# Kernel optimization log

Measured on AMD Instinct MI355X. Metric: run time of the kernel, lower is better.

Reference implementation:

```python
import jax, jax.numpy as jnp
import numpy as np

B, S, H, D = 2, 2048, 16, 64
HID = H * D
THETA = 10000.0
SCALING_FACTOR = 1
NEG_INF = -1e9


def _rope_cos_sin(position_ids):
    # Llama RoPE: inv_freq over even dims, duplicated halves.
    inv_freq = 1.0 / (THETA ** (jnp.arange(0, D, 2, dtype=jnp.float32) / D))  # [D/2]
    freqs = position_ids.astype(jnp.float32)[..., None] * inv_freq            # [B,S,D/2]
    emb = jnp.concatenate([freqs, freqs], axis=-1)                            # [B,S,D]
    return jnp.cos(emb), jnp.sin(emb)


def _rotate_half(x):
    x1, x2 = jnp.split(x, 2, axis=-1)
    return jnp.concatenate([-x2, x1], axis=-1)


def setup_inputs() -> dict:
    key = jax.random.key(0)
    ks = jax.random.split(key, 6)
    return {
        "hidden_states": jax.random.normal(ks[0], (B, S, HID), dtype=jnp.float32),
        "info_embeddings": jax.random.normal(ks[1], (B, S, HID), dtype=jnp.float32) * 0.1,
        "Wq": jax.random.normal(ks[2], (HID, HID), dtype=jnp.float32) * 0.02,
        "Wk": jax.random.normal(ks[3], (HID, HID), dtype=jnp.float32) * 0.02,
        "Wv": jax.random.normal(ks[4], (HID, HID), dtype=jnp.float32) * 0.02,
        "Wo": jax.random.normal(ks[5], (HID, HID), dtype=jnp.float32) * 0.02,
        "position_ids": jnp.broadcast_to(jnp.arange(S, dtype=jnp.int64), (B, S)),
    }


def reference(hidden_states, info_embeddings, Wq, Wk, Wv, Wo, position_ids):
    b, s, _ = hidden_states.shape
    # projections -> [B,H,S,D]
    q = (hidden_states @ Wq).reshape(b, s, H, D).transpose(0, 2, 1, 3)
    k = (hidden_states @ Wk).reshape(b, s, H, D).transpose(0, 2, 1, 3)
    v = (hidden_states @ Wv).reshape(b, s, H, D).transpose(0, 2, 1, 3)
    # info embedding added to q and k (pre-RoPE)
    info = info_embeddings.reshape(b, s, H, D).transpose(0, 2, 1, 3)
    q = q + info
    k = k + info
    # rotary position embedding
    cos, sin = _rope_cos_sin(position_ids)
    cos = cos[:, None]  # [B,1,S,D]
    sin = sin[:, None]
    q = q * cos + _rotate_half(q) * sin
    k = k * cos + _rotate_half(k) * sin
    # eager attention with custom scaling
    scale = 1.0 / float(np.sqrt(SCALING_FACTOR * D))
    scores = jnp.einsum("bhqd,bhkd->bhqk", q, k) * scale  # [B,H,S,S]
    causal = jnp.tril(jnp.ones((s, s), dtype=bool))
    scores = scores + jnp.where(causal, 0.0, NEG_INF).astype(scores.dtype)
    probs = jax.nn.softmax(scores, axis=-1)  # dropout p=0 (eval)
    attn = jnp.einsum("bhqk,bhkd->bhqd", probs, v)
    attn = attn.transpose(0, 2, 1, 3).reshape(b, s, HID)
    return attn @ Wo
```

## Files before the change

kernel.cpp:

```cpp
#include <hip/hip_runtime.h>
#include <hip/hip_bf16.h>

#define HB 2
#define HS 2048
#define HH 16
#define HD 64
#define HIDN 1024
#define MROWS 4096

typedef __attribute__((ext_vector_type(8))) short s16x8;
typedef __attribute__((ext_vector_type(4))) float f32x4;
typedef unsigned short u16;

__device__ inline u16 f2bf(float f) {
  union { __hip_bfloat16 h; u16 u; } cvt;
  cvt.h = __float2bfloat16(f);
  return cvt.u;
}

__global__ __launch_bounds__(256) void k_cvt(const float* __restrict__ in, u16* __restrict__ out, int n) {
  int i = (blockIdx.x * 256 + threadIdx.x) * 4;
  if (i >= n) return;
  float4 a = *(const float4*)(in + i);
  ushort4 r;
  r.x = f2bf(a.x); r.y = f2bf(a.y); r.z = f2bf(a.z); r.w = f2bf(a.w);
  *(ushort4*)(out + i) = r;
}

__global__ __launch_bounds__(256) void k_transpose(const float* __restrict__ W0, const float* __restrict__ W1,
                                                   const float* __restrict__ W2, const float* __restrict__ W3,
                                                   u16* __restrict__ out) {
  const float* W = (blockIdx.z == 0) ? W0 : (blockIdx.z == 1) ? W1 : (blockIdx.z == 2) ? W2 : W3;
  u16* O = out + (size_t)blockIdx.z * HIDN * HIDN;
  __shared__ float tile[64][65];
  int k0 = blockIdx.y * 64, c0 = blockIdx.x * 64;
  #pragma unroll
  for (int i = 0; i < 16; ++i) {
    int id = threadIdx.x + i * 256;
    int r = id >> 6, c = id & 63;
    tile[r][c] = W[(size_t)(k0 + r) * HIDN + c0 + c];
  }
  __syncthreads();
  #pragma unroll
  for (int i = 0; i < 16; ++i) {
    int id = threadIdx.x + i * 256;
    int r = id >> 6, c = id & 63;
    O[(size_t)(c0 + r) * HIDN + k0 + c] = f2bf(tile[c][r]);
  }
}

#define BM 128
#define BN 128
#define BK 64
#define LDK 72

__global__ __launch_bounds__(256) void k_qkv(const u16* __restrict__ X, const u16* __restrict__ Wt,
                                             const float* __restrict__ info,
                                             u16* __restrict__ Qb, u16* __restrict__ Kb, u16* __restrict__ Vt) {
  __shared__ u16 As[BM * LDK];
  __shared__ u16 Bs[BN * LDK];
  const int z = blockIdx.z;
  const u16* Bt = Wt + (size_t)z * HIDN * HIDN;
  const int tid = threadIdx.x;
  const int lane = tid & 63, wave = tid >> 6;
  const int wr = wave >> 1, wc = wave & 1;
  const int lg = lane >> 4, li = lane & 15;
  const int bm0 = blockIdx.y * BM, bn0 = blockIdx.x * BN;

  f32x4 acc[4][4];
  #pragma unroll
  for (int m = 0; m < 4; ++m)
    #pragma unroll
    for (int n = 0; n < 4; ++n) acc[m][n] = (f32x4){0.f, 0.f, 0.f, 0.f};

  for (int k0 = 0; k0 < HIDN; k0 += BK) {
    __syncthreads();
    #pragma unroll
    for (int i = 0; i < 4; ++i) {
      int id = tid + i * 256;
      int r = id >> 3, kc = (id & 7) * 8;
      *(uint4*)(&As[r * LDK + kc]) = *(const uint4*)(X  + (size_t)(bm0 + r) * HIDN + k0 + kc);
      *(uint4*)(&Bs[r * LDK + kc]) = *(const uint4*)(Bt + (size_t)(bn0 + r) * HIDN + k0 + kc);
    }
    __syncthreads();
    #pragma unroll
    for (int kk = 0; kk < 2; ++kk) {
      s16x8 af[4], bfr[4];
      #pragma unroll
      for (int m = 0; m < 4; ++m) af[m]  = *(const s16x8*)(&As[(wr * 64 + m * 16 + li) * LDK + kk * 32 + lg * 8]);
      #pragma unroll
      for (int n = 0; n < 4; ++n) bfr[n] = *(const s16x8*)(&Bs[(wc * 64 + n * 16 + li) * LDK + kk * 32 + lg * 8]);
      #pragma unroll
      for (int m = 0; m < 4; ++m)
        #pragma unroll
        for (int n = 0; n < 4; ++n)
          acc[m][n] = __builtin_amdgcn_mfma_f32_16x16x32_bf16(af[m], bfr[n], acc[m][n], 0, 0, 0);
    }
  }

  if (z < 2) {
    u16* dst = (z == 0) ? Qb : Kb;
    #pragma unroll
    for (int m = 0; m < 4; ++m) {
      #pragma unroll
      for (int r = 0; r < 4; ++r) {
        int t = bm0 + wr * 64 + m * 16 + lg * 4 + r;
        int b = t >> 11, s = t & (HS - 1);
        #pragma unroll
        for (int n = 0; n < 2; ++n) {
          int c1 = bn0 + wc * 64 + n * 16 + li;
          float v1 = acc[m][n][r]     + info[(size_t)t * HIDN + c1];
          float v2 = acc[m][n + 2][r] + info[(size_t)t * HIDN + c1 + 32];
          int j = n * 16 + li;
          float invf = exp2f(-0.41524101186092030f * (float)j);
          float ang = (float)s * invf;
          float sn, cs;
          __sincosf(ang, &sn, &cs);
          float o1 = v1 * cs - v2 * sn;
          float o2 = v2 * cs + v1 * sn;
          if (z == 0) { o1 *= 0.18033688011f; o2 *= 0.18033688011f; }
          int h = c1 >> 6, d1 = c1 & 63;
          size_t base = ((size_t)(b * HH + h) * HS + s) * HD;
          dst[base + d1]      = f2bf(o1);
          dst[base + d1 + 32] = f2bf(o2);
        }
      }
    }
  } else {
    #pragma unroll
    for (int m = 0; m < 4; ++m) {
      #pragma unroll
      for (int r = 0; r < 4; ++r) {
        int t = bm0 + wr * 64 + m * 16 + lg * 4 + r;
        int b = t >> 11, s = t & (HS - 1);
        #pragma unroll
        for (int n = 0; n < 4; ++n) {
          int c = bn0 + wc * 64 + n * 16 + li;
          int h = c >> 6, d = c & 63;
          Vt[((size_t)(b * HH + h) * HD + d) * HS + s] = f2bf(acc[m][n][r]);
        }
      }
    }
  }
}

__global__ __launch_bounds__(256) void k_attn(const u16* __restrict__ Qb, const u16* __restrict__ Kb,
                                              const u16* __restrict__ Vt, u16* __restrict__ attnOut) {
  __shared__ u16 Ks[64 * LDK];
  __shared__ u16 Vs[64 * LDK];
  __shared__ u16 Ps[4][16 * LDK];
  const int bh = blockIdx.y;
  const u16* Qh = Qb + (size_t)bh * HS * HD;
  const u16* Kh = Kb + (size_t)bh * HS * HD;
  const u16* Vh = Vt + (size_t)bh * HD * HS;
  const int tid = threadIdx.x;
  const int lane = tid & 63, wave = tid >> 6;
  const int lg = lane >> 4, li = lane & 15;
  const int b = bh >> 4, h = bh & 15;

  const int sr0 = tid >> 3,          sc0 = (tid & 7) * 8;
  const int sr1 = (tid + 256) >> 3,  sc1 = ((tid + 256) & 7) * 8;

  #pragma unroll
  for (int phase = 0; phase < 2; ++phase) {
    const int qt = (phase == 0) ? (31 - (int)blockIdx.x) : (int)blockIdx.x;
    const int q0 = qt * 64;
    const int ntiles = qt + 1;

    s16x8 qf[2];
    #pragma unroll
    for (int kk = 0; kk < 2; ++kk)
      qf[kk] = *(const s16x8*)(Qh + (size_t)(q0 + wave * 16 + li) * HD + kk * 32 + lg * 8);

    f32x4 o[4];
    #pragma unroll
    for (int n = 0; n < 4; ++n) o[n] = (f32x4){0.f, 0.f, 0.f, 0.f};
    float mrow = -3e38f, lrow = 0.f;

    uint4 rK0, rK1, rV0, rV1;
    rK0 = *(const uint4*)(Kh + (size_t)sr0 * HD + sc0);
    rK1 = *(const uint4*)(Kh + (size_t)sr1 * HD + sc1);
    rV0 = *(const uint4*)(Vh + (size_t)sr0 * HS + sc0);
    rV1 = *(const uint4*)(Vh + (size_t)sr1 * HS + sc1);

    for (int t = 0; t < ntiles; ++t) {
      __syncthreads();
      *(uint4*)(&Ks[sr0 * LDK + sc0]) = rK0;
      *(uint4*)(&Ks[sr1 * LDK + sc1]) = rK1;
      *(uint4*)(&Vs[sr0 * LDK + sc0]) = rV0;
      *(uint4*)(&Vs[sr1 * LDK + sc1]) = rV1;
      __syncthreads();
      if (t + 1 < ntiles) {
        const int kv1 = (t + 1) * 64;
        rK0 = *(const uint4*)(Kh + (size_t)(kv1 + sr0) * HD + sc0);
        rK1 = *(const uint4*)(Kh + (size_t)(kv1 + sr1) * HD + sc1);
        rV0 = *(const uint4*)(Vh + (size_t)sr0 * HS + kv1 + sc0);
        rV1 = *(const uint4*)(Vh + (size_t)sr1 * HS + kv1 + sc1);
      }

      f32x4 sc[4];
      #pragma unroll
      for (int n = 0; n < 4; ++n) sc[n] = (f32x4){0.f, 0.f, 0.f, 0.f};
      __builtin_amdgcn_s_setprio(1);
      #pragma unroll
      for (int kk = 0; kk < 2; ++kk) {
        #pragma unroll
        for (int n = 0; n < 4; ++n) {
          s16x8 kfr = *(const s16x8*)(&Ks[(n * 16 + li) * LDK + kk * 32 + lg * 8]);
          sc[n] = __builtin_amdgcn_mfma_f32_16x16x32_bf16(kfr, qf[kk], sc[n], 0, 0, 0);
        }
      }
      __builtin_amdgcn_s_setprio(0);

      if (t == ntiles - 1) {
        const int qrel = wave * 16 + li;
        #pragma unroll
        for (int n = 0; n < 4; ++n)
          #pragma unroll
          for (int r = 0; r < 4; ++r)
            if (n * 16 + lg * 4 + r > qrel) sc[n][r] = -1e9f;
      }

      float pmax = sc[0][0];
      #pragma unroll
      for (int n = 0; n < 4; ++n)
        #pragma unroll
        for (int r = 0; r < 4; ++r) pmax = fmaxf(pmax, sc[n][r]);
      pmax = fmaxf(pmax, __shfl_xor(pmax, 16));
      pmax = fmaxf(pmax, __shfl_xor(pmax, 32));

      if (!__all(pmax - mrow <= 11.5f)) {
        float mnew = fmaxf(mrow, pmax);
        float corr = exp2f(mrow - mnew);
        mrow = mnew;
        lrow *= corr;
        float corrq[4];
        #pragma unroll
        for (int r = 0; r < 4; ++r) corrq[r] = __shfl(corr, lg * 4 + r);
        #pragma unroll
        for (int n = 0; n < 4; ++n)
          #pragma unroll
          for (int r = 0; r < 4; ++r) o[n][r] *= corrq[r];
      }

      float psum = 0.f;
      #pragma unroll
      for (int n = 0; n < 4; ++n) {
        u16 pb[4];
        #pragma unroll
        for (int r = 0; r < 4; ++r) {
          float p = exp2f(sc[n][r] - mrow);
          psum += p;
          pb[r] = f2bf(p);
        }
        uint2 w;
        w.x = (unsigned)pb[0] | ((unsigned)pb[1] << 16);
        w.y = (unsigned)pb[2] | ((unsigned)pb[3] << 16);
        *(uint2*)(&Ps[wave][li * LDK + n * 16 + lg * 4]) = w;
      }
      psum += __shfl_xor(psum, 16);
      psum += __shfl_xor(psum, 32);
      lrow += psum;

      __builtin_amdgcn_s_setprio(1);
      #pragma unroll
      for (int kk = 0; kk < 2; ++kk) {
        s16x8 pf = *(const s16x8*)(&Ps[wave][li * LDK + kk * 32 + lg * 8]);
        #pragma unroll
        for (int n = 0; n < 4; ++n) {
          s16x8 vf = *(const s16x8*)(&Vs[(n * 16 + li) * LDK + kk * 32 + lg * 8]);
          o[n] = __builtin_amdgcn_mfma_f32_16x16x32_bf16(pf, vf, o[n], 0, 0, 0);
        }
      }
      __builtin_amdgcn_s_setprio(0);
    }

    float linv = 1.0f / lrow;
    float linvq[4];
    #pragma unroll
    for (int r = 0; r < 4; ++r) linvq[r] = __shfl(linv, lg * 4 + r);
    #pragma unroll
    for (int n = 0; n < 4; ++n)
      #pragma unroll
      for (int r = 0; r < 4; ++r) {
        int srow = q0 + wave * 16 + lg * 4 + r;
        attnOut[(size_t)(b * HS + srow) * HIDN + h * 64 + n * 16 + li] = f2bf(o[n][r] * linvq[r]);
      }
  }
}

__global__ __launch_bounds__(256) void k_out(const u16* __restrict__ A, const u16* __restrict__ Bt,
                                             float* __restrict__ out) {
  __shared__ u16 As[BM * LDK];
  __shared__ u16 Bs[BN * LDK];
  const int tid = threadIdx.x;
  const int lane = tid & 63, wave = tid >> 6;
  const int wr = wave >> 1, wc = wave & 1;
  const int lg = lane >> 4, li = lane & 15;
  const int bm0 = blockIdx.y * BM, bn0 = blockIdx.x * BN;

  f32x4 acc[4][4];
  #pragma unroll
  for (int m = 0; m < 4; ++m)
    #pragma unroll
    for (int n = 0; n < 4; ++n) acc[m][n] = (f32x4){0.f, 0.f, 0.f, 0.f};

  for (int k0 = 0; k0 < HIDN; k0 += BK) {
    __syncthreads();
    #pragma unroll
    for (int i = 0; i < 4; ++i) {
      int id = tid + i * 256;
      int r = id >> 3, kc = (id & 7) * 8;
      *(uint4*)(&As[r * LDK + kc]) = *(const uint4*)(A  + (size_t)(bm0 + r) * HIDN + k0 + kc);
      *(uint4*)(&Bs[r * LDK + kc]) = *(const uint4*)(Bt + (size_t)(bn0 + r) * HIDN + k0 + kc);
    }
    __syncthreads();
    #pragma unroll
    for (int kk = 0; kk < 2; ++kk) {
      s16x8 af[4], bfr[4];
      #pragma unroll
      for (int m = 0; m < 4; ++m) af[m]  = *(const s16x8*)(&As[(wr * 64 + m * 16 + li) * LDK + kk * 32 + lg * 8]);
      #pragma unroll
      for (int n = 0; n < 4; ++n) bfr[n] = *(const s16x8*)(&Bs[(wc * 64 + n * 16 + li) * LDK + kk * 32 + lg * 8]);
      #pragma unroll
      for (int m = 0; m < 4; ++m)
        #pragma unroll
        for (int n = 0; n < 4; ++n)
          acc[m][n] = __builtin_amdgcn_mfma_f32_16x16x32_bf16(af[m], bfr[n], acc[m][n], 0, 0, 0);
    }
  }

  #pragma unroll
  for (int m = 0; m < 4; ++m)
    #pragma unroll
    for (int r = 0; r < 4; ++r) {
      int t = bm0 + wr * 64 + m * 16 + lg * 4 + r;
      #pragma unroll
      for (int n = 0; n < 4; ++n) {
        int c = bn0 + wc * 64 + n * 16 + li;
        out[(size_t)t * HIDN + c] = acc[m][n][r];
      }
    }
}

extern "C" void kernel_launch(void* const* d_in, const int* in_sizes, int n_in,
                              void* d_out, int out_size, void* d_ws, size_t ws_size,
                              hipStream_t stream) {
  const float* hs   = (const float*)d_in[0];
  const float* info = (const float*)d_in[1];
  const float* Wq   = (const float*)d_in[2];
  const float* Wk   = (const float*)d_in[3];
  const float* Wv   = (const float*)d_in[4];
  const float* Wo   = (const float*)d_in[5];
  float* out = (float*)d_out;

  char* ws = (char*)d_ws;
  u16* Xbf  = (u16*)(ws);
  u16* Wt   = (u16*)(ws + ((size_t)8  << 20));
  u16* Qb   = (u16*)(ws + ((size_t)16 << 20));
  u16* Kb   = (u16*)(ws + ((size_t)24 << 20));
  u16* Vt   = (u16*)(ws + ((size_t)32 << 20));
  u16* attn = Xbf;

  k_cvt<<<(MROWS * HIDN / 4 + 255) / 256, 256, 0, stream>>>(hs, Xbf, MROWS * HIDN);
  k_transpose<<<dim3(16, 16, 4), 256, 0, stream>>>(Wq, Wk, Wv, Wo, Wt);
  k_qkv<<<dim3(HIDN / BN, MROWS / BM, 3), 256, 0, stream>>>(Xbf, Wt, info, Qb, Kb, Vt);
  k_attn<<<dim3(16, HB * HH), 256, 0, stream>>>(Qb, Kb, Vt, attn);
  k_out<<<dim3(HIDN / BN, MROWS / BM), 256, 0, stream>>>(attn, Wt + (size_t)3 * HIDN * HIDN, out);
}
```

Before: 133.5 us.

## Use direct global-to-LDS loads in GEMMs and stage V transpose through LDS

Both GEMM kernels now load tiles with global_load_lds, which writes straight into unpadded LDS rows and skips the round trip through registers. The MFMA blocks are wrapped in s_setprio to favour the math waves. The V epilogue now transposes the tile through shared memory and writes contiguous 16-byte vectors, replacing scattered 2-byte stores. The unpadded 64-element row stride may cause LDS bank conflicts on the fragment reads.

Result: faster. 127.5 us (-4.5%).

```diff
diff --git a/kernel.cpp b/kernel.cpp
--- a/kernel.cpp
+++ b/kernel.cpp
@@ -16,6 +16,11 @@
   union { __hip_bfloat16 h; u16 u; } cvt;
   cvt.h = __float2bfloat16(f);
   return cvt.u;
+}
+
+__device__ __forceinline__ void gload16(const u16* g, u16* l) {
+  __builtin_amdgcn_global_load_lds((const __attribute__((address_space(1))) void*)g,
+                                   (__attribute__((address_space(3))) void*)l, 16, 0, 0);
 }
 
 __global__ __launch_bounds__(256) void k_cvt(const float* __restrict__ in, u16* __restrict__ out, int n) {
@@ -57,8 +62,7 @@
 __global__ __launch_bounds__(256) void k_qkv(const u16* __restrict__ X, const u16* __restrict__ Wt,
                                              const float* __restrict__ info,
                                              u16* __restrict__ Qb, u16* __restrict__ Kb, u16* __restrict__ Vt) {
-  __shared__ u16 As[BM * LDK];
-  __shared__ u16 Bs[BN * LDK];
+  __shared__ __align__(16) u16 smem[128 * 136];
   const int z = blockIdx.z;
   const u16* Bt = Wt + (size_t)z * HIDN * HIDN;
   const int tid = threadIdx.x;
@@ -67,6 +71,9 @@
   const int lg = lane >> 4, li = lane & 15;
   const int bm0 = blockIdx.y * BM, bn0 = blockIdx.x * BN;
 
+  const int srow = lane >> 3;
+  const int scol = (lane & 7) * 8;
+
   f32x4 acc[4][4];
   #pragma unroll
   for (int m = 0; m < 4; ++m)
@@ -76,25 +83,27 @@
   for (int k0 = 0; k0 < HIDN; k0 += BK) {
     __syncthreads();
     #pragma unroll
-    for (int i = 0; i < 4; ++i) {
-      int id = tid + i * 256;
-      int r = id >> 3, kc = (id & 7) * 8;
-      *(uint4*)(&As[r * LDK + kc]) = *(const uint4*)(X  + (size_t)(bm0 + r) * HIDN + k0 + kc);
-      *(uint4*)(&Bs[r * LDK + kc]) = *(const uint4*)(Bt + (size_t)(bn0 + r) * HIDN + k0 + kc);
+    for (int c = 0; c < 4; ++c) {
+      const int ci = wave * 4 + c;
+      const int row = ci * 8 + srow;
+      gload16(X  + (size_t)(bm0 + row) * HIDN + k0 + scol, &smem[ci * 512]);
+      gload16(Bt + (size_t)(bn0 + row) * HIDN + k0 + scol, &smem[8192 + ci * 512]);
     }
     __syncthreads();
     #pragma unroll
     for (int kk = 0; kk < 2; ++kk) {
       s16x8 af[4], bfr[4];
       #pragma unroll
-      for (int m = 0; m < 4; ++m) af[m]  = *(const s16x8*)(&As[(wr * 64 + m * 16 + li) * LDK + kk * 32 + lg * 8]);
-      #pragma unroll
-      for (int n = 0; n < 4; ++n) bfr[n] = *(const s16x8*)(&Bs[(wc * 64 + n * 16 + li) * LDK + kk * 32 + lg * 8]);
+      for (int m = 0; m < 4; ++m) af[m]  = *(const s16x8*)(&smem[(wr * 64 + m * 16 + li) * 64 + kk * 32 + lg * 8]);
+      #pragma unroll
+      for (int n = 0; n < 4; ++n) bfr[n] = *(const s16x8*)(&smem[8192 + (wc * 64 + n * 16 + li) * 64 + kk * 32 + lg * 8]);
+      __builtin_amdgcn_s_setprio(1);
       #pragma unroll
       for (int m = 0; m < 4; ++m)
         #pragma unroll
         for (int n = 0; n < 4; ++n)
           acc[m][n] = __builtin_amdgcn_mfma_f32_16x16x32_bf16(af[m], bfr[n], acc[m][n], 0, 0, 0);
+      __builtin_amdgcn_s_setprio(0);
     }
   }
 
@@ -127,19 +136,27 @@
       }
     }
   } else {
-    #pragma unroll
-    for (int m = 0; m < 4; ++m) {
-      #pragma unroll
-      for (int r = 0; r < 4; ++r) {
-        int t = bm0 + wr * 64 + m * 16 + lg * 4 + r;
-        int b = t >> 11, s = t & (HS - 1);
-        #pragma unroll
-        for (int n = 0; n < 4; ++n) {
-          int c = bn0 + wc * 64 + n * 16 + li;
-          int h = c >> 6, d = c & 63;
-          Vt[((size_t)(b * HH + h) * HD + d) * HS + s] = f2bf(acc[m][n][r]);
-        }
-      }
+    __syncthreads();
+    #pragma unroll
+    for (int m = 0; m < 4; ++m)
+      #pragma unroll
+      for (int n = 0; n < 4; ++n)
+        #pragma unroll
+        for (int r = 0; r < 4; ++r) {
+          int cl = wc * 64 + n * 16 + li;
+          int ml = wr * 64 + m * 16 + lg * 4 + r;
+          smem[cl * 136 + ml] = f2bf(acc[m][n][r]);
+        }
+    __syncthreads();
+    const int b = bm0 >> 11, s0 = bm0 & (HS - 1);
+    #pragma unroll
+    for (int p = 0; p < 8; ++p) {
+      int id = tid + p * 256;
+      int cl = id >> 4, m8 = (id & 15) * 8;
+      int c = bn0 + cl;
+      int h = c >> 6, d = c & 63;
+      s16x8 v = *(const s16x8*)(&smem[cl * 136 + m8]);
+      *(s16x8*)(&Vt[((size_t)(b * HH + h) * HD + d) * HS + s0 + m8]) = v;
     }
   }
 }
@@ -291,14 +308,17 @@
 
 __global__ __launch_bounds__(256) void k_out(const u16* __restrict__ A, const u16* __restrict__ Bt,
                                              float* __restrict__ out) {
-  __shared__ u16 As[BM * LDK];
-  __shared__ u16 Bs[BN * LDK];
+  __shared__ __align__(16) u16 As[BM * 64];
+  __shared__ __align__(16) u16 Bs[BN * 64];
   const int tid = threadIdx.x;
   const int lane = tid & 63, wave = tid >> 6;
   const int wr = wave >> 1, wc = wave & 1;
   const int lg = lane >> 4, li = lane & 15;
   const int bm0 = blockIdx.y * BM, bn0 = blockIdx.x * BN;
 
+  const int srow = lane >> 3;
+  const int scol = (lane & 7) * 8;
+
   f32x4 acc[4][4];
   #pragma unroll
   for (int m = 0; m < 4; ++m)
@@ -308,25 +328,27 @@
   for (int k0 = 0; k0 < HIDN; k0 += BK) {
     __syncthreads();
     #pragma unroll
-    for (int i = 0; i < 4; ++i) {
-      int id = tid + i * 256;
-      int r = id >> 3, kc = (id & 7) * 8;
-      *(uint4*)(&As[r * LDK + kc]) = *(const uint4*)(A  + (size_t)(bm0 + r) * HIDN + k0 + kc);
-      *(uint4*)(&Bs[r * LDK + kc]) = *(const uint4*)(Bt + (size_t)(bn0 + r) * HIDN + k0 + kc);
+    for (int c = 0; c < 4; ++c) {
+      const int ci = wave * 4 + c;
+      const int row = ci * 8 + srow;
+      gload16(A  + (size_t)(bm0 + row) * HIDN + k0 + scol, &As[ci * 512]);
+      gload16(Bt + (size_t)(bn0 + row) * HIDN + k0 + scol, &Bs[ci * 512]);
     }
     __syncthreads();
     #pragma unroll
     for (int kk = 0; kk < 2; ++kk) {
       s16x8 af[4], bfr[4];
       #pragma unroll
-      for (int m = 0; m < 4; ++m) af[m]  = *(const s16x8*)(&As[(wr * 64 + m * 16 + li) * LDK + kk * 32 + lg * 8]);
-      #pragma unroll
-      for (int n = 0; n < 4; ++n) bfr[n] = *(const s16x8*)(&Bs[(wc * 64 + n * 16 + li) * LDK + kk * 32 + lg * 8]);
+      for (int m = 0; m < 4; ++m) af[m]  = *(const s16x8*)(&As[(wr * 64 + m * 16 + li) * 64 + kk * 32 + lg * 8]);
+      #pragma unroll
+      for (int n = 0; n < 4; ++n) bfr[n] = *(const s16x8*)(&Bs[(wc * 64 + n * 16 + li) * 64 + kk * 32 + lg * 8]);
+      __builtin_amdgcn_s_setprio(1);
       #pragma unroll
       for (int m = 0; m < 4; ++m)
         #pragma unroll
         for (int n = 0; n < 4; ++n)
           acc[m][n] = __builtin_amdgcn_mfma_f32_16x16x32_bf16(af[m], bfr[n], acc[m][n], 0, 0, 0);
+      __builtin_amdgcn_s_setprio(0);
     }
   }
 
```
